# Performance work log

Measured on AMD Instinct MI355X. Metric: run time of the kernel, lower is better.

The kernel has to match this reference:

```python
import jax, jax.numpy as jnp
import numpy as np

NUM_CAPSULE = 16
DIM_CAPSULE = 32
ROUTINGS = 4
EPS = 1e-07


def squash(x, axis=-1):
    # NOTE: faithful to the source: x / sqrt(sum(x^2) + eps) (unit-norm style),
    # NOT the standard Hinton squash.
    s2 = jnp.sum(x * x, axis=axis, keepdims=True)
    return x / jnp.sqrt(s2 + EPS)


def setup_inputs() -> dict:
    key = jax.random.key(0)
    k1, k2 = jax.random.split(key)
    B, N_in, D_in = 128, 1024, 256
    x = jax.random.normal(k1, (B, N_in, D_in), dtype=jnp.float32)
    # xavier_normal over (1, D_in, NUM_CAPSULE*DIM_CAPSULE)
    fan_in, fan_out = D_in, NUM_CAPSULE * DIM_CAPSULE
    std = np.sqrt(2.0 / (fan_in + fan_out))
    W = jax.random.normal(k2, (1, D_in, NUM_CAPSULE * DIM_CAPSULE), dtype=jnp.float32) * std
    return {"x": x, "W": W}


def reference(x, W):
    B, N_in, _ = x.shape
    # u_hat: [B, N_in, num_cap*dim_cap] -> [B, num_cap, N_in, dim_cap]
    u_hat = jnp.matmul(x, W[0])
    u_hat = u_hat.reshape(B, N_in, NUM_CAPSULE, DIM_CAPSULE).transpose(0, 2, 1, 3)

    b = jnp.zeros((B, NUM_CAPSULE, N_in), dtype=u_hat.dtype)
    outputs = None
    for i in range(ROUTINGS):
        # torch permutes to softmax over the num_capsule axis; equivalent to axis=1 here
        c = jax.nn.softmax(b, axis=1)                      # [B, num_cap, N_in]
        outputs = squash(jnp.einsum('bij,bijk->bik', c, u_hat))  # [B, num_cap, dim_cap]
        if i < ROUTINGS - 1:
            b = jnp.einsum('bik,bijk->bij', outputs, u_hat)
    return outputs
```

## Files before the change

### kernel.cpp

```cpp
#include <hip/hip_runtime.h>

typedef unsigned int u32;
typedef unsigned short u16;
typedef float f32x4 __attribute__((ext_vector_type(4)));
typedef __bf16 bf16x8 __attribute__((ext_vector_type(8)));

#define BATCH 128
#define NIN   1024
#define DIN   256
#define NC    16
#define DC    32
#define NCOL  512

__device__ __forceinline__ float bflo(u32 v){ return __uint_as_float(v << 16); }
__device__ __forceinline__ float bfhi(u32 v){ return __uint_as_float(v & 0xffff0000u); }
__device__ __forceinline__ u32 bfround(u32 ua){ return (ua + 0x7fffu + ((ua >> 16) & 1u)) >> 16; }
__device__ __forceinline__ u32 pack2(float a, float b){
    return (bfround(__float_as_uint(a)) & 0xffffu) | (bfround(__float_as_uint(b)) << 16);
}
__device__ __forceinline__ bf16x8 ldfrag(const u16* p){
    return __builtin_bit_cast(bf16x8, *(const uint4*)p);
}

__device__ __forceinline__ int lds_x(int r, int d){
    int sw = (d >> 2) ^ ((r & 7) << 1) ^ (((r >> 3) & 3) << 2);
    return r * 256 + (sw << 2) + (d & 3);
}

__global__ __launch_bounds__(256) void k_pre(const float* __restrict__ x, const float* __restrict__ W,
                                             u16* __restrict__ xb, float* __restrict__ s,
                                             uint2* __restrict__ Wb, uint2* __restrict__ WT){
    const int t = threadIdx.x, seg = blockIdx.x, b = blockIdx.y;

    if (seg == 0){
        int id = b * 256 + t;
        float4 w4 = ((const float4*)W)[id];
        Wb[id] = make_uint2(pack2(w4.x, w4.y), pack2(w4.z, w4.w));
        int c = id >> 6, d4 = id & 63;
        float e0 = W[(size_t)(d4 * 4 + 0) * NCOL + c];
        float e1 = W[(size_t)(d4 * 4 + 1) * NCOL + c];
        float e2 = W[(size_t)(d4 * 4 + 2) * NCOL + c];
        float e3 = W[(size_t)(d4 * 4 + 3) * NCOL + c];
        WT[c * 64 + d4] = make_uint2(pack2(e0, e1), pack2(e2, e3));
    }
    const float4* xg = (const float4*)(x + ((size_t)b * NIN + seg * 64) * DIN);
    uint2* xbw = (uint2*)xb + ((size_t)(b * NIN + seg * 64)) * 64;
    int d4 = t & 63, r0 = t >> 6;
    float cs0 = 0.f, cs1 = 0.f, cs2 = 0.f, cs3 = 0.f;
    #pragma unroll
    for (int m = 0; m < 16; m++){
        int r = r0 + 4 * m;
        float4 v = xg[r * 64 + d4];
        uint2 p = make_uint2(pack2(v.x, v.y), pack2(v.z, v.w));
        xbw[r * 64 + d4] = p;
        cs0 += bflo(p.x); cs1 += bfhi(p.x);
        cs2 += bflo(p.y); cs3 += bfhi(p.y);
    }
    atomicAdd(&s[b * DIN + d4 * 4 + 0], cs0);
    atomicAdd(&s[b * DIN + d4 * 4 + 1], cs1);
    atomicAdd(&s[b * DIN + d4 * 4 + 2], cs2);
    atomicAdd(&s[b * DIN + d4 * 4 + 3], cs3);
}

__global__ __launch_bounds__(256) void k_main(const u16* __restrict__ xb, const u16* __restrict__ vb,
                                              float* __restrict__ zg){
    __shared__ __align__(16) u16 xt[128 * 256];
    __shared__ float bbl[16][132];
    __shared__ __align__(16) u16 cl[16][136];
    const int t = threadIdx.x, jh = blockIdx.x, b = blockIdx.y;
    const int lane = t & 63, wv = t >> 6;
    const int l15 = lane & 15, q = lane >> 4;

    uint4 vf[8];
    #pragma unroll
    for (int ks = 0; ks < 8; ks++)
        vf[ks] = *(const uint4*)&vb[((size_t)b * 16 + l15) * 256 + ks * 32 + q * 8];

    {
        const uint4* xg = (const uint4*)(xb + ((size_t)(b * NIN + jh * 128)) * 256);
        #pragma unroll
        for (int m = 0; m < 16; m++){
            int id = t + 256 * m;
            int row = id >> 5, c8 = id & 31;
            uint4 v = xg[id];
            *(uint4*)&xt[lds_x(row, c8 * 8)] = v;
        }
    }
    __syncthreads();

    #pragma unroll
    for (int u = 0; u < 2; u++){
        int jt = wv * 2 + u;
        f32x4 acc = {0.f, 0.f, 0.f, 0.f};
        #pragma unroll
        for (int ks = 0; ks < 8; ks++)
            acc = __builtin_amdgcn_mfma_f32_16x16x32_bf16(
                __builtin_bit_cast(bf16x8, vf[ks]),
                ldfrag(&xt[lds_x(jt * 16 + l15, ks * 32 + q * 8)]), acc, 0, 0, 0);
        #pragma unroll
        for (int r = 0; r < 4; r++) bbl[q * 4 + r][jt * 16 + l15] = acc[r];
    }
    __syncthreads();

    if (t < 128){
        float mx = -1e30f, e[16], sum = 0.f;
        #pragma unroll
        for (int i = 0; i < 16; i++) mx = fmaxf(mx, bbl[i][t]);
        #pragma unroll
        for (int i = 0; i < 16; i++){ e[i] = __expf(bbl[i][t] - mx); sum += e[i]; }
        float inv = 1.f / sum;
        #pragma unroll
        for (int i = 0; i < 16; i++) cl[i][t] = (u16)bfround(__float_as_uint(e[i] * inv));
    }
    __syncthreads();

    #pragma unroll
    for (int u = 0; u < 4; u++){
        int dt = wv * 4 + u;
        f32x4 acc = {0.f, 0.f, 0.f, 0.f};
        #pragma unroll
        for (int js = 0; js < 4; js++){
            u32 w[4];
            #pragma unroll
            for (int e2 = 0; e2 < 4; e2++){
                u32 lo = xt[lds_x(js * 32 + q * 8 + 2 * e2,     dt * 16 + l15)];
                u32 hi = xt[lds_x(js * 32 + q * 8 + 2 * e2 + 1, dt * 16 + l15)];
                w[e2] = lo | (hi << 16);
            }
            bf16x8 cf = ldfrag(&cl[l15][js * 32 + q * 8]);
            acc = __builtin_amdgcn_mfma_f32_16x16x32_bf16(
                cf, __builtin_bit_cast(bf16x8, make_uint4(w[0], w[1], w[2], w[3])), acc, 0, 0, 0);
        }
        #pragma unroll
        for (int r = 0; r < 4; r++)
            atomicAdd(&zg[((size_t)b * 16 + q * 4 + r) * 256 + dt * 16 + l15], acc[r]);
    }
}

__global__ __launch_bounds__(256) void k_tail(const float* __restrict__ s, float* __restrict__ zg,
                                              const u16* __restrict__ Wb, const u32* __restrict__ WT32,
                                              u16* __restrict__ vb, float* __restrict__ out, int mode){
    __shared__ float zl[8][260];
    __shared__ __align__(16) float ol[256];
    const int ih2 = blockIdx.x, b = blockIdx.y, t = threadIdx.x;
    const int i_loc = t >> 5;
    const int o_idx = ih2 * 256 + t;
    float y = 0.f;
    if (mode == 0){
        zl[0][t] = s[b * 256 + t] * (1.f / 16.f);
        __syncthreads();
        #pragma unroll 8
        for (int d = 0; d < 256; d++) y += zl[0][d] * bflo((u32)Wb[d * 512 + o_idx]);
    } else {
        #pragma unroll
        for (int u0 = 0; u0 < 8; u0++){
            int idx = t + 256 * u0;
            int ii = idx >> 8, dd = idx & 255;
            size_t a = ((size_t)b * 16 + ih2 * 8 + ii) * 256 + dd;
            float acc = zg[a];
            if (mode == 1) zg[a] = 0.f;
            zl[ii][dd] = acc;
        }
        __syncthreads();
        #pragma unroll 8
        for (int d = 0; d < 256; d++) y += zl[i_loc][d] * bflo((u32)Wb[d * 512 + o_idx]);
    }
    float s2 = y * y;
    s2 += __shfl_xor(s2, 1); s2 += __shfl_xor(s2, 2); s2 += __shfl_xor(s2, 4);
    s2 += __shfl_xor(s2, 8); s2 += __shfl_xor(s2, 16);
    float r = y / sqrtf(s2 + 1e-7f);
    if (mode == 2){ out[b * 512 + o_idx] = r; return; }
    ol[t] = r;
    __syncthreads();
    {
        int dh = t & 127, ihalf = t >> 7;
        #pragma unroll
        for (int e = 0; e < 4; e++){
            int ii = ihalf * 4 + e;
            int i2 = ih2 * 8 + ii;
            float a0 = 0.f, a1 = 0.f;
            #pragma unroll
            for (int k = 0; k < 32; k++){
                u32 wv2 = WT32[(size_t)(i2 * 32 + k) * 128 + dh];
                float ok = ol[ii * 32 + k];
                a0 += ok * bflo(wv2); a1 += ok * bfhi(wv2);
            }
            ((u32*)vb)[(size_t)(b * 16 + i2) * 128 + dh] = pack2(a0, a1);
        }
    }
}

extern "C" void kernel_launch(void* const* d_in, const int* in_sizes, int n_in,
                              void* d_out, int out_size, void* d_ws, size_t ws_size,
                              hipStream_t stream){
    const float* x = (const float*)d_in[0];
    const float* W = (const float*)d_in[1];
    float* out = (float*)d_out;
    char* ws = (char*)d_ws;
    float* s    = (float*)(ws);
    float* zg   = (float*)(ws + 131072);
    u16*   Wb   = (u16*)  (ws + 2228224);
    u32*   WT   = (u32*)  (ws + 2490368);
    u16*   vb   = (u16*)  (ws + 2752512);
    u16*   xb   = (u16*)  (ws + 3801088);

    hipMemsetAsync(ws, 0, 2228224, stream);
    k_pre<<<dim3(16, BATCH), 256, 0, stream>>>(x, W, xb, s, (uint2*)Wb, (uint2*)WT);
    k_tail<<<dim3(2, BATCH), 256, 0, stream>>>(s, zg, Wb, WT, vb, out, 0);
    for (int it = 1; it < 4; it++){
        k_main<<<dim3(8, BATCH), 256, 0, stream>>>(xb, vb, zg);
        k_tail<<<dim3(2, BATCH), 256, 0, stream>>>(s, zg, Wb, WT, vb, out, it == 3 ? 2 : 1);
    }
}
```

Before: 341.7 us.

## Halve k_main tile to 64 rows with 512 threads, split-K logits, LDS-reduce pre sums

```diff
diff --git a/kernel.cpp b/kernel.cpp
--- a/kernel.cpp
+++ b/kernel.cpp
@@ -30,9 +30,10 @@
 __global__ __launch_bounds__(256) void k_pre(const float* __restrict__ x, const float* __restrict__ W,
                                              u16* __restrict__ xb, float* __restrict__ s,
                                              uint2* __restrict__ Wb, uint2* __restrict__ WT){
-    const int t = threadIdx.x, seg = blockIdx.x, b = blockIdx.y;
-
-    if (seg == 0){
+    __shared__ float csum[4][256];
+    const int t = threadIdx.x, jc = blockIdx.x, b = blockIdx.y;
+
+    if (jc == 0){
         int id = b * 256 + t;
         float4 w4 = ((const float4*)W)[id];
         Wb[id] = make_uint2(pack2(w4.x, w4.y), pack2(w4.z, w4.w));
@@ -43,83 +44,94 @@
         float e3 = W[(size_t)(d4 * 4 + 3) * NCOL + c];
         WT[c * 64 + d4] = make_uint2(pack2(e0, e1), pack2(e2, e3));
     }
-    const float4* xg = (const float4*)(x + ((size_t)b * NIN + seg * 64) * DIN);
-    uint2* xbw = (uint2*)xb + ((size_t)(b * NIN + seg * 64)) * 64;
-    int d4 = t & 63, r0 = t >> 6;
+    const float4* xg = (const float4*)(x + ((size_t)b * NIN + jc * 64) * DIN);
+    uint2* xbw = (uint2*)xb + ((size_t)(b * NIN + jc * 64)) * 64;
     float cs0 = 0.f, cs1 = 0.f, cs2 = 0.f, cs3 = 0.f;
     #pragma unroll
-    for (int m = 0; m < 16; m++){
-        int r = r0 + 4 * m;
-        float4 v = xg[r * 64 + d4];
-        uint2 p = make_uint2(pack2(v.x, v.y), pack2(v.z, v.w));
-        xbw[r * 64 + d4] = p;
-        cs0 += bflo(p.x); cs1 += bfhi(p.x);
-        cs2 += bflo(p.y); cs3 += bfhi(p.y);
-    }
-    atomicAdd(&s[b * DIN + d4 * 4 + 0], cs0);
-    atomicAdd(&s[b * DIN + d4 * 4 + 1], cs1);
-    atomicAdd(&s[b * DIN + d4 * 4 + 2], cs2);
-    atomicAdd(&s[b * DIN + d4 * 4 + 3], cs3);
-}
-
-__global__ __launch_bounds__(256) void k_main(const u16* __restrict__ xb, const u16* __restrict__ vb,
+    for (int mb = 0; mb < 2; mb++){
+        float4 v[8];
+        #pragma unroll
+        for (int m = 0; m < 8; m++) v[m] = xg[mb * 2048 + t + 256 * m];
+        #pragma unroll
+        for (int m = 0; m < 8; m++){
+            uint2 p = make_uint2(pack2(v[m].x, v[m].y), pack2(v[m].z, v[m].w));
+            xbw[mb * 2048 + t + 256 * m] = p;
+            cs0 += bflo(p.x); cs1 += bfhi(p.x);
+            cs2 += bflo(p.y); cs3 += bfhi(p.y);
+        }
+    }
+    *(float4*)&csum[t >> 6][(t & 63) * 4] = make_float4(cs0, cs1, cs2, cs3);
+    __syncthreads();
+    {
+        float acc = csum[0][t] + csum[1][t] + csum[2][t] + csum[3][t];
+        atomicAdd(&s[b * DIN + t], acc);
+    }
+}
+
+__global__ __launch_bounds__(512) void k_main(const u16* __restrict__ xb, const u16* __restrict__ vb,
                                               float* __restrict__ zg){
-    __shared__ __align__(16) u16 xt[128 * 256];
-    __shared__ float bbl[16][132];
-    __shared__ __align__(16) u16 cl[16][136];
-    const int t = threadIdx.x, jh = blockIdx.x, b = blockIdx.y;
+    __shared__ __align__(16) u16 xt[64 * 256];
+    __shared__ float bbl[2][16][68];
+    __shared__ __align__(16) u16 cl[16][80];
+    const int t = threadIdx.x, jc = blockIdx.x, b = blockIdx.y;
     const int lane = t & 63, wv = t >> 6;
     const int l15 = lane & 15, q = lane >> 4;
-
-    uint4 vf[8];
-    #pragma unroll
-    for (int ks = 0; ks < 8; ks++)
-        vf[ks] = *(const uint4*)&vb[((size_t)b * 16 + l15) * 256 + ks * 32 + q * 8];
-
-    {
-        const uint4* xg = (const uint4*)(xb + ((size_t)(b * NIN + jh * 128)) * 256);
-        #pragma unroll
-        for (int m = 0; m < 16; m++){
-            int id = t + 256 * m;
-            int row = id >> 5, c8 = id & 31;
-            uint4 v = xg[id];
-            *(uint4*)&xt[lds_x(row, c8 * 8)] = v;
-        }
-    }
-    __syncthreads();
-
+    const int kh = wv >> 2, jt = wv & 3;
+
+    uint4 st[4];
+    {
+        const uint4* xg = (const uint4*)(xb + ((size_t)(b * NIN + jc * 64)) * 256);
+        #pragma unroll
+        for (int m = 0; m < 4; m++) st[m] = xg[t + 512 * m];
+    }
+    uint4 vf[4];
+    #pragma unroll
+    for (int e = 0; e < 4; e++)
+        vf[e] = *(const uint4*)&vb[((size_t)b * 16 + l15) * 256 + (kh * 4 + e) * 32 + q * 8];
+    #pragma unroll
+    for (int m = 0; m < 4; m++){
+        int id = t + 512 * m;
+        *(uint4*)&xt[lds_x(id >> 5, (id & 31) * 8)] = st[m];
+    }
+    __syncthreads();
+
+    {
+        f32x4 acc = {0.f, 0.f, 0.f, 0.f};
+        #pragma unroll
+        for (int e = 0; e < 4; e++)
+            acc = __builtin_amdgcn_mfma_f32_16x16x32_bf16(
+                __builtin_bit_cast(bf16x8, vf[e]),
+                ldfrag(&xt[lds_x(jt * 16 + l15, (kh * 4 + e) * 32 + q * 8)]), acc, 0, 0, 0);
+        #pragma unroll
+        for (int r = 0; r < 4; r++) bbl[kh][q * 4 + r][jt * 16 + l15] = acc[r];
+    }
+    __syncthreads();
+
+    if (t < 64){
+        float mx = -1e30f, e[16], sum = 0.f;
+        #pragma unroll
+        for (int i = 0; i < 16; i++){
+            float v = bbl[0][i][t] + bbl[1][i][t];
+            bbl[0][i][t] = v;
+            mx = fmaxf(mx, v);
+        }
+        #pragma unroll
+        for (int i = 0; i < 16; i++){ e[i] = __expf(bbl[0][i][t] - mx); sum += e[i]; }
+        float inv = 1.f / sum;
+        #pragma unroll
+        for (int i = 0; i < 16; i++) cl[i][t] = (u16)bfround(__float_as_uint(e[i] * inv));
+    }
+    __syncthreads();
+
+    bf16x8 cf[2];
+    #pragma unroll
+    for (int js = 0; js < 2; js++) cf[js] = ldfrag(&cl[l15][js * 32 + q * 8]);
     #pragma unroll
     for (int u = 0; u < 2; u++){
-        int jt = wv * 2 + u;
+        int dt = wv * 2 + u;
         f32x4 acc = {0.f, 0.f, 0.f, 0.f};
         #pragma unroll
-        for (int ks = 0; ks < 8; ks++)
-            acc = __builtin_amdgcn_mfma_f32_16x16x32_bf16(
-                __builtin_bit_cast(bf16x8, vf[ks]),
-                ldfrag(&xt[lds_x(jt * 16 + l15, ks * 32 + q * 8)]), acc, 0, 0, 0);
-        #pragma unroll
-        for (int r = 0; r < 4; r++) bbl[q * 4 + r][jt * 16 + l15] = acc[r];
-    }
-    __syncthreads();
-
-    if (t < 128){
-        float mx = -1e30f, e[16], sum = 0.f;
-        #pragma unroll
-        for (int i = 0; i < 16; i++) mx = fmaxf(mx, bbl[i][t]);
-        #pragma unroll
-        for (int i = 0; i < 16; i++){ e[i] = __expf(bbl[i][t] - mx); sum += e[i]; }
-        float inv = 1.f / sum;
-        #pragma unroll
-        for (int i = 0; i < 16; i++) cl[i][t] = (u16)bfround(__float_as_uint(e[i] * inv));
-    }
-    __syncthreads();
-
-    #pragma unroll
-    for (int u = 0; u < 4; u++){
-        int dt = wv * 4 + u;
-        f32x4 acc = {0.f, 0.f, 0.f, 0.f};
-        #pragma unroll
-        for (int js = 0; js < 4; js++){
+        for (int js = 0; js < 2; js++){
             u32 w[4];
             #pragma unroll
             for (int e2 = 0; e2 < 4; e2++){
@@ -127,9 +139,8 @@
                 u32 hi = xt[lds_x(js * 32 + q * 8 + 2 * e2 + 1, dt * 16 + l15)];
                 w[e2] = lo | (hi << 16);
             }
-            bf16x8 cf = ldfrag(&cl[l15][js * 32 + q * 8]);
             acc = __builtin_amdgcn_mfma_f32_16x16x32_bf16(
-                cf, __builtin_bit_cast(bf16x8, make_uint4(w[0], w[1], w[2], w[3])), acc, 0, 0, 0);
+                cf[js], __builtin_bit_cast(bf16x8, make_uint4(w[0], w[1], w[2], w[3])), acc, 0, 0, 0);
         }
         #pragma unroll
         for (int r = 0; r < 4; r++)
@@ -208,7 +219,7 @@
     k_pre<<<dim3(16, BATCH), 256, 0, stream>>>(x, W, xb, s, (uint2*)Wb, (uint2*)WT);
     k_tail<<<dim3(2, BATCH), 256, 0, stream>>>(s, zg, Wb, WT, vb, out, 0);
     for (int it = 1; it < 4; it++){
-        k_main<<<dim3(8, BATCH), 256, 0, stream>>>(xb, vb, zg);
+        k_main<<<dim3(16, BATCH), 512, 0, stream>>>(xb, vb, zg);
         k_tail<<<dim3(2, BATCH), 256, 0, stream>>>(s, zg, Wb, WT, vb, out, it == 3 ? 2 : 1);
     }
 }
```

Result: slower. 373.3 us (+9.2%).
